# Kernel optimization log

Hardware: AMD Instinct MI355X
Metric: run time of the kernel (lower is better)

Reference implementation:

```python
import jax, jax.numpy as jnp
import numpy as np

B, L, PHYS, D = 1024, 1024, 2, 16


def setup_inputs() -> dict:
    key = jax.random.key(0)
    k1, k2 = jax.random.split(key)
    # local quantum numbers s_i in {0,1} (spin-1/2), already normalized
    x = jax.random.randint(k1, (B, L), 0, PHYS, dtype=jnp.int32)
    # kernel = identity + small noise, as in setup() (param + iden_tensors)
    noise = 0.01 * jax.random.normal(k2, (L, PHYS, D, D), dtype=jnp.float32)
    kernel = noise + jnp.eye(D, dtype=jnp.float32)
    return {"x": x, "kernel": kernel}


def reference(x, kernel):
    # kernel: [L, phys, D, D]; x: [B, L] int local states (bias=0, spacing=1)
    Lc = kernel.shape[0]
    Dd = kernel.shape[-1]
    Bb = x.shape[0]
    # gather the MPS tensor at each site for each configuration -> [B, L, D, D]
    selected = kernel[jnp.arange(Lc)[None, :], x]
    # sequential matrix-chain product over the chain, batched over B
    ts = jnp.swapaxes(selected, 0, 1)  # [L, B, D, D]
    init = jnp.broadcast_to(jnp.eye(Dd, dtype=kernel.dtype), (Bb, Dd, Dd))

    def step(carry, t):
        return jnp.einsum('bij,bjk->bik', carry, t), None

    final, _ = jax.lax.scan(step, init, ts)  # [B, D, D]
    return jnp.log(jnp.trace(final, axis1=-2, axis2=-1))  # [B]
```

## Files before the change

### kernel.cpp

```cpp
#include <hip/hip_runtime.h>
#include <math.h>

#define LL 1024
#define BB 1024
#define NCHUNK4 256
#define SEGS 8
#define STEPS 32
#define RST 20
#define SLOT20 328

typedef float f32x4 __attribute__((ext_vector_type(4)));
typedef short s16x8 __attribute__((ext_vector_type(8)));

#define FMA4(acc, s, v) { (acc).x += (s)*(v).x; (acc).y += (s)*(v).y; \
                          (acc).z += (s)*(v).z; (acc).w += (s)*(v).w; }

__device__ inline unsigned f2bf(float f) {
    unsigned u = __float_as_uint(f);
    return (u + 0x7FFFu + ((u >> 16) & 1u)) >> 16;
}

__device__ inline void mulRST(float* L, int sx, int sy, int sd, int sub) {
    const int q = sub >> 4, j = sub & 15;
    const float* X = &L[sx*SLOT20 + j*RST];
    const float* Y = &L[sy*SLOT20 + 4*q];
    float4 o = make_float4(0.f, 0.f, 0.f, 0.f);
    #pragma unroll
    for (int i = 0; i < 16; ++i) {
        const float a = X[i];
        const float4 y = *reinterpret_cast<const float4*>(Y + i*RST);
        FMA4(o, a, y);
    }
    *reinterpret_cast<float4*>(&L[sd*SLOT20 + j*RST + 4*q]) = o;
}

__global__ __launch_bounds__(256) void build_frag3(const float* __restrict__ km,
                                                   uint2* __restrict__ TA) {
    const int blk = blockIdx.x;
    const int c   = blk >> 2;
    const int m01 = blk & 3;
    const int xs0 = m01 >> 1, xs1 = m01 & 1;
    const int t = threadIdx.x;
    __shared__ float L[13 * SLOT20];

    const int dst = (t >> 4)*RST + (t & 15);
    L[0*SLOT20 + dst] = km[((4*c + 0)*2 + xs0)*256 + t];
    L[1*SLOT20 + dst] = km[((4*c + 1)*2 + xs1)*256 + t];
    L[2*SLOT20 + dst] = km[((4*c + 2)*2 + 0)*256 + t];
    L[3*SLOT20 + dst] = km[((4*c + 2)*2 + 1)*256 + t];
    L[4*SLOT20 + dst] = km[((4*c + 3)*2 + 0)*256 + t];
    L[5*SLOT20 + dst] = km[((4*c + 3)*2 + 1)*256 + t];
    __syncthreads();

    const int w = t >> 6, sub = t & 63;
    if (w == 0) mulRST(L, 0, 1, 6, sub);
    __syncthreads();
    if (w < 2) mulRST(L, 6, 2 + w, 7 + w, sub);
    __syncthreads();
    mulRST(L, 7 + (w >> 1), 4 + (w & 1), 9 + w, sub);
    __syncthreads();

    {
        const int g = sub >> 4, col = sub & 15;
        const float* Tq = &L[(9 + w) * SLOT20];
        const unsigned a0 = f2bf(Tq[(4*g+0)*RST + col]);
        const unsigned a1 = f2bf(Tq[(4*g+1)*RST + col]);
        const unsigned a2 = f2bf(Tq[(4*g+2)*RST + col]);
        const unsigned a3 = f2bf(Tq[(4*g+3)*RST + col]);
        TA[((size_t)c*16 + m01*4 + w)*64 + sub] =
            make_uint2(a0 | (a1 << 16), a2 | (a3 << 16));
    }
}

__global__ __launch_bounds__(512) void mps_fused(const uint2* __restrict__ TA,
                                                 const int* __restrict__ x,
                                                 float* __restrict__ out) {
    __shared__ float mats[12 * SLOT20];
    const int tt   = threadIdx.x;
    const int b    = blockIdx.x;
    const int s    = tt >> 6;
    const int lane = tt & 63;
    const int g = lane >> 4, c = lane & 15;

    int mv = 0;
    {
        const int4* xp4 = reinterpret_cast<const int4*>(x + (size_t)b*LL + s*(STEPS*4));
        if (lane < STEPS) {
            const int4 xv = xp4[lane];
            mv = (xv.x<<3) | (xv.y<<2) | (xv.z<<1) | xv.w;
        }
    }
    const uint2* __restrict__ TAs = TA + (size_t)s*STEPS*16*64;

    const f32x4 zero = {0.f, 0.f, 0.f, 0.f};
    f32x4 d = zero;
    unsigned h01 = ((4*g+0==c)?0x3F80u:0u) | (((4*g+1==c)?0x3F80u:0u) << 16);
    unsigned h23 = ((4*g+2==c)?0x3F80u:0u) | (((4*g+3==c)?0x3F80u:0u) << 16);
    unsigned l01 = 0u, l23 = 0u;

    #pragma unroll
    for (int t = 0; t < STEPS; ++t) {
        const int ms = __builtin_amdgcn_readlane(mv, t);
        const uint2 av = TAs[((size_t)t*16 + ms)*64 + lane];
        union { uint4 u; s16x8 v; } ua, ub;
        ua.u = make_uint4(av.x, av.y, av.x, av.y);
        ub.u = make_uint4(h01, h23, l01, l23);
        d = __builtin_amdgcn_mfma_f32_16x16x32_bf16(ua.v, ub.v, zero, 0, 0, 0);
        asm("v_cvt_pk_bf16_f32 %0, %1, %2" : "=v"(h01) : "v"(d[0]), "v"(d[1]));
        asm("v_cvt_pk_bf16_f32 %0, %1, %2" : "=v"(h23) : "v"(d[2]), "v"(d[3]));
        const float r0 = d[0] - __uint_as_float(h01 << 16);
        const float r1 = d[1] - __uint_as_float(h01 & 0xFFFF0000u);
        const float r2 = d[2] - __uint_as_float(h23 << 16);
        const float r3 = d[3] - __uint_as_float(h23 & 0xFFFF0000u);
        asm("v_cvt_pk_bf16_f32 %0, %1, %2" : "=v"(l01) : "v"(r0), "v"(r1));
        asm("v_cvt_pk_bf16_f32 %0, %1, %2" : "=v"(l23) : "v"(r2), "v"(r3));
    }
    #pragma unroll
    for (int j = 0; j < 4; ++j) mats[s*SLOT20 + (4*g+j)*RST + c] = d[j];
    __syncthreads();

    if (tt < 256) mulRST(mats, 2*s + 1, 2*s, 8 + s, lane);
    __syncthreads();
    if (tt < 128) mulRST(mats, 8 + 2*s + 1, 8 + 2*s, s, lane);
    __syncthreads();
    if (tt < 64) mulRST(mats, 1, 0, 2, lane);
    __syncthreads();

    if (tt < 16) {
        float dg = mats[2*SLOT20 + tt*RST + tt];
        #pragma unroll
        for (int off = 8; off >= 1; off >>= 1) dg += __shfl_xor(dg, off, 16);
        if (tt == 0) out[b] = logf(dg);
    }
}

__global__ void seg_prod1(const float* __restrict__ T, const int* __restrict__ x,
                          float* __restrict__ P, const int S, const int lgS) {
    const int tid  = blockIdx.x * blockDim.x + threadIdx.x;
    const int j    = tid & 15;
    const int item = tid >> 4;
    if (item >= BB * S) return;
    const int s = item & (S - 1);
    const int b = item >> lgS;
    float c[16];
    #pragma unroll
    for (int q = 0; q < 16; ++q) c[q] = (q == j) ? 1.f : 0.f;
    const int nsteps = LL / S;
    const int base   = s * nsteps;
    for (int cc = 0; cc < nsteps; ++cc) {
        const int l = base + cc;
        const int xv = x[(size_t)b*LL + l];
        const float4* Mrow = reinterpret_cast<const float4*>(T + ((size_t)l*2 + xv)*256);
        float4 n0 = make_float4(0.f,0.f,0.f,0.f), n1 = n0, n2 = n0, n3 = n0;
        #pragma unroll
        for (int i = 0; i < 16; ++i) {
            const float a = c[i];
            const float4 r0 = Mrow[i*4+0], r1 = Mrow[i*4+1], r2 = Mrow[i*4+2], r3 = Mrow[i*4+3];
            FMA4(n0, a, r0); FMA4(n1, a, r1); FMA4(n2, a, r2); FMA4(n3, a, r3);
        }
        c[0]=n0.x; c[1]=n0.y; c[2]=n0.z; c[3]=n0.w;
        c[4]=n1.x; c[5]=n1.y; c[6]=n1.z; c[7]=n1.w;
        c[8]=n2.x; c[9]=n2.y; c[10]=n2.z; c[11]=n2.w;
        c[12]=n3.x; c[13]=n3.y; c[14]=n3.z; c[15]=n3.w;
    }
    float4* Pp = reinterpret_cast<float4*>(P + (size_t)item*256 + j*16);
    Pp[0] = make_float4(c[0],c[1],c[2],c[3]);
    Pp[1] = make_float4(c[4],c[5],c[6],c[7]);
    Pp[2] = make_float4(c[8],c[9],c[10],c[11]);
    Pp[3] = make_float4(c[12],c[13],c[14],c[15]);
}

__global__ void combine_gen(const float* __restrict__ P, float* __restrict__ out,
                            const int S) {
    const int g = threadIdx.x >> 4;
    const int j = threadIdx.x & 15;
    const int b = blockIdx.x * 4 + g;
    float c[16];
    {
        const float4* p0 = reinterpret_cast<const float4*>(P + (size_t)(b*S)*256 + j*16);
        const float4 v0 = p0[0], v1 = p0[1], v2 = p0[2], v3 = p0[3];
        c[0]=v0.x; c[1]=v0.y; c[2]=v0.z; c[3]=v0.w;
        c[4]=v1.x; c[5]=v1.y; c[6]=v1.z; c[7]=v1.w;
        c[8]=v2.x; c[9]=v2.y; c[10]=v2.z; c[11]=v2.w;
        c[12]=v3.x; c[13]=v3.y; c[14]=v3.z; c[15]=v3.w;
    }
    for (int s = 1; s < S; ++s) {
        const float4* Mrow = reinterpret_cast<const float4*>(P + (size_t)(b*S + s)*256);
        float4 n0 = make_float4(0.f,0.f,0.f,0.f), n1 = n0, n2 = n0, n3 = n0;
        #pragma unroll
        for (int i = 0; i < 16; ++i) {
            const float a = c[i];
            const float4 r0 = Mrow[i*4+0], r1 = Mrow[i*4+1], r2 = Mrow[i*4+2], r3 = Mrow[i*4+3];
            FMA4(n0, a, r0); FMA4(n1, a, r1); FMA4(n2, a, r2); FMA4(n3, a, r3);
        }
        c[0]=n0.x; c[1]=n0.y; c[2]=n0.z; c[3]=n0.w;
        c[4]=n1.x; c[5]=n1.y; c[6]=n1.z; c[7]=n1.w;
        c[8]=n2.x; c[9]=n2.y; c[10]=n2.z; c[11]=n2.w;
        c[12]=n3.x; c[13]=n3.y; c[14]=n3.z; c[15]=n3.w;
    }
    float diag = 0.f;
    #pragma unroll
    for (int k = 0; k < 16; ++k) diag = (k == j) ? c[k] : diag;
    #pragma unroll
    for (int off = 8; off >= 1; off >>= 1) diag += __shfl_xor(diag, off, 16);
    if (j == 0) out[b] = logf(diag);
}

extern "C" void kernel_launch(void* const* d_in, const int* in_sizes, int n_in,
                              void* d_out, int out_size, void* d_ws, size_t ws_size,
                              hipStream_t stream) {
    const int*   x  = (const int*)d_in[0];
    const float* km = (const float*)d_in[1];
    float* out = (float*)d_out;

    const size_t tab = (size_t)NCHUNK4 * 16 * 64 * sizeof(uint2);

    if (ws_size >= tab) {
        uint2* TA = (uint2*)d_ws;
        build_frag3<<<NCHUNK4*4, 256, 0, stream>>>(km, TA);
        mps_fused<<<BB, 512, 0, stream>>>(TA, x, out);
    } else {
        int S = 16;
        while (S > 1 && (size_t)BB * S * 256 * sizeof(float) > ws_size) S >>= 1;
        int lgS = 0; for (int t = S; t > 1; t >>= 1) ++lgS;
        float* P = (float*)d_ws;
        const int blocks = (BB*S*16 + 255) / 256;
        seg_prod1<<<blocks, 256, 0, stream>>>(km, x, P, S, lgS);
        combine_gen<<<BB/4, 64, 0, stream>>>(P, out, S);
    }
}
```

Baseline: 22.81 us.

## Fuse table build and chain kernels into one cooperative launch with grid sync

Merges the table-building kernel and the chain-product kernel into a single cooperative kernel that builds the bf16 fragment table, then does a grid-wide sync before running the chain phase. The aim is to remove the second kernel launch and the gap between the two dispatches. It requires all 1024 blocks of 512 threads to be co-resident, and adds an occupancy query on every call plus the cost of the grid barrier. If the occupancy check fails, it falls back to the two-kernel path.

```diff
diff --git a/kernel.cpp b/kernel.cpp
--- a/kernel.cpp
+++ b/kernel.cpp
@@ -1,5 +1,8 @@
 #include <hip/hip_runtime.h>
+#include <hip/hip_cooperative_groups.h>
 #include <math.h>
+
+namespace cg = cooperative_groups;
 
 #define LL 1024
 #define BB 1024
@@ -34,33 +37,29 @@
     *reinterpret_cast<float4*>(&L[sd*SLOT20 + j*RST + 4*q]) = o;
 }
 
-__global__ __launch_bounds__(256) void build_frag3(const float* __restrict__ km,
-                                                   uint2* __restrict__ TA) {
-    const int blk = blockIdx.x;
-    const int c   = blk >> 2;
-    const int m01 = blk & 3;
+__device__ inline void build_phase(float* L, const float* __restrict__ km,
+                                   uint2* __restrict__ TA, int bid, int tt) {
+    const int c   = bid >> 2;
+    const int m01 = bid & 3;
     const int xs0 = m01 >> 1, xs1 = m01 & 1;
-    const int t = threadIdx.x;
-    __shared__ float L[13 * SLOT20];
-
-    const int dst = (t >> 4)*RST + (t & 15);
-    L[0*SLOT20 + dst] = km[((4*c + 0)*2 + xs0)*256 + t];
-    L[1*SLOT20 + dst] = km[((4*c + 1)*2 + xs1)*256 + t];
-    L[2*SLOT20 + dst] = km[((4*c + 2)*2 + 0)*256 + t];
-    L[3*SLOT20 + dst] = km[((4*c + 2)*2 + 1)*256 + t];
-    L[4*SLOT20 + dst] = km[((4*c + 3)*2 + 0)*256 + t];
-    L[5*SLOT20 + dst] = km[((4*c + 3)*2 + 1)*256 + t];
-    __syncthreads();
-
-    const int w = t >> 6, sub = t & 63;
+    if (tt < 256) {
+        const int dst = (tt >> 4)*RST + (tt & 15);
+        L[0*SLOT20 + dst] = km[((4*c + 0)*2 + xs0)*256 + tt];
+        L[1*SLOT20 + dst] = km[((4*c + 1)*2 + xs1)*256 + tt];
+        L[2*SLOT20 + dst] = km[((4*c + 2)*2 + 0)*256 + tt];
+        L[3*SLOT20 + dst] = km[((4*c + 2)*2 + 1)*256 + tt];
+        L[4*SLOT20 + dst] = km[((4*c + 3)*2 + 0)*256 + tt];
+        L[5*SLOT20 + dst] = km[((4*c + 3)*2 + 1)*256 + tt];
+    }
+    __syncthreads();
+    const int w = tt >> 6, sub = tt & 63;
     if (w == 0) mulRST(L, 0, 1, 6, sub);
     __syncthreads();
     if (w < 2) mulRST(L, 6, 2 + w, 7 + w, sub);
     __syncthreads();
-    mulRST(L, 7 + (w >> 1), 4 + (w & 1), 9 + w, sub);
-    __syncthreads();
-
-    {
+    if (w < 4) mulRST(L, 7 + (w >> 1), 4 + (w & 1), 9 + w, sub);
+    __syncthreads();
+    if (tt < 256) {
         const int g = sub >> 4, col = sub & 15;
         const float* Tq = &L[(9 + w) * SLOT20];
         const unsigned a0 = f2bf(Tq[(4*g+0)*RST + col]);
@@ -72,12 +71,9 @@
     }
 }
 
-__global__ __launch_bounds__(512) void mps_fused(const uint2* __restrict__ TA,
-                                                 const int* __restrict__ x,
-                                                 float* __restrict__ out) {
-    __shared__ float mats[12 * SLOT20];
-    const int tt   = threadIdx.x;
-    const int b    = blockIdx.x;
+__device__ inline void chain_phase(float* mats, const uint2* __restrict__ TA,
+                                   const int* __restrict__ x,
+                                   float* __restrict__ out, int b, int tt) {
     const int s    = tt >> 6;
     const int lane = tt & 63;
     const int g = lane >> 4, c = lane & 15;
@@ -123,7 +119,7 @@
     __syncthreads();
     if (tt < 128) mulRST(mats, 8 + 2*s + 1, 8 + 2*s, s, lane);
     __syncthreads();
-    if (tt < 64) mulRST(mats, 1, 0, 2, lane);
+    if (tt < 64)  mulRST(mats, 1, 0, 2, lane);
     __syncthreads();
 
     if (tt < 16) {
@@ -132,6 +128,32 @@
         for (int off = 8; off >= 1; off >>= 1) dg += __shfl_xor(dg, off, 16);
         if (tt == 0) out[b] = logf(dg);
     }
+}
+
+__global__ __launch_bounds__(512, 8) void mps_all(const float* __restrict__ km,
+                                                  const int* __restrict__ x,
+                                                  uint2* __restrict__ TA,
+                                                  float* __restrict__ out) {
+    __shared__ float L[13 * SLOT20];
+    const int tt  = threadIdx.x;
+    const int bid = blockIdx.x;
+    build_phase(L, km, TA, bid, tt);
+    __threadfence();
+    cg::this_grid().sync();
+    chain_phase(L, TA, x, out, bid, tt);
+}
+
+__global__ __launch_bounds__(256) void build_frag3(const float* __restrict__ km,
+                                                   uint2* __restrict__ TA) {
+    __shared__ float L[13 * SLOT20];
+    build_phase(L, km, TA, blockIdx.x, threadIdx.x);
+}
+
+__global__ __launch_bounds__(512) void mps_fused(const uint2* __restrict__ TA,
+                                                 const int* __restrict__ x,
+                                                 float* __restrict__ out) {
+    __shared__ float mats[12 * SLOT20];
+    chain_phase(mats, TA, x, out, blockIdx.x, threadIdx.x);
 }
 
 __global__ void seg_prod1(const float* __restrict__ T, const int* __restrict__ x,
@@ -217,8 +239,17 @@
 
     if (ws_size >= tab) {
         uint2* TA = (uint2*)d_ws;
-        build_frag3<<<NCHUNK4*4, 256, 0, stream>>>(km, TA);
-        mps_fused<<<BB, 512, 0, stream>>>(TA, x, out);
+        int nb = 0;
+        hipError_t qe = hipOccupancyMaxActiveBlocksPerMultiprocessor(
+            &nb, (const void*)mps_all, 512, 0);
+        if (qe == hipSuccess && nb >= 4) {
+            void* args[] = { (void*)&km, (void*)&x, (void*)&TA, (void*)&out };
+            hipLaunchCooperativeKernel((const void*)mps_all, dim3(BB), dim3(512),
+                                       args, 0, stream);
+        } else {
+            build_frag3<<<NCHUNK4*4, 256, 0, stream>>>(km, TA);
+            mps_fused<<<BB, 512, 0, stream>>>(TA, x, out);
+        }
     } else {
         int S = 16;
         while (S > 1 && (size_t)BB * S * 256 * sizeof(float) > ws_size) S >>= 1;
```

After: 28.61 us. 25.4% more time.
